# Optimization experiments

Hardware: AMD Instinct MI355X
Metric: run time of the kernel (lower is better)

Reference implementation:

```python
import jax, jax.numpy as jnp
import numpy as np

N_ATOMS = 100000
N_BONDS = 400000
ATOM_FDIM = 133
BOND_FDIM = 147
HIDDEN = 300
DEPTH = 3


def setup_inputs() -> dict:
    key = jax.random.key(0)
    ks = jax.random.split(key, 10)
    f_atoms = jax.random.normal(ks[0], (N_ATOMS, ATOM_FDIM), dtype=jnp.float32)
    f_bonds = jax.random.normal(ks[1], (N_BONDS, BOND_FDIM), dtype=jnp.float32)
    b2a = jax.random.randint(ks[2], (N_BONDS,), 0, N_ATOMS)
    b2revb = jax.random.randint(ks[3], (N_BONDS,), 0, N_BONDS)
    s_i = 1.0 / np.sqrt(BOND_FDIM)
    s_h = 1.0 / np.sqrt(HIDDEN)
    s_o = 1.0 / np.sqrt(ATOM_FDIM + HIDDEN)
    Wi_w = jax.random.uniform(ks[4], (HIDDEN, BOND_FDIM), jnp.float32, -s_i, s_i)
    Wi_b = jax.random.uniform(ks[5], (HIDDEN,), jnp.float32, -s_i, s_i)
    Wh_w = jax.random.uniform(ks[6], (HIDDEN, HIDDEN), jnp.float32, -s_h, s_h)
    Wh_b = jax.random.uniform(ks[7], (HIDDEN,), jnp.float32, -s_h, s_h)
    Wo_w = jax.random.uniform(ks[8], (HIDDEN, ATOM_FDIM + HIDDEN), jnp.float32, -s_o, s_o)
    Wo_b = jax.random.uniform(ks[9], (HIDDEN,), jnp.float32, -s_o, s_o)
    return {"f_atoms": f_atoms, "f_bonds": f_bonds, "b2a": b2a, "b2revb": b2revb,
            "Wi_w": Wi_w, "Wi_b": Wi_b, "Wh_w": Wh_w, "Wh_b": Wh_b,
            "Wo_w": Wo_w, "Wo_b": Wo_b}


def reference(f_atoms, f_bonds, b2a, b2revb, Wi_w, Wi_b, Wh_w, Wh_b, Wo_w, Wo_b):
    n_atoms = f_atoms.shape[0]
    # initial bond messages: [n_bonds, hidden]
    H_bonds = jax.nn.relu(f_bonds @ Wi_w.T + Wi_b)
    dest = b2a[b2revb]  # destination atom of each directed bond
    for _ in range(DEPTH - 1):
        # scatter-add bond messages onto destination atoms
        sum_msgs = jax.ops.segment_sum(H_bonds, dest, num_segments=n_atoms)
        # gather back to bonds from source atoms, subtract reverse-bond message
        msgs = sum_msgs[b2a] - H_bonds[b2revb]
        H_bonds = jax.nn.relu(H_bonds + msgs @ Wh_w.T + Wh_b)
    sum_msgs = jax.ops.segment_sum(H_bonds, dest, num_segments=n_atoms)
    H_atoms = jax.nn.relu(jnp.concatenate([f_atoms, sum_msgs], axis=1) @ Wo_w.T + Wo_b)
    return (H_atoms, H_bonds)
```

## Files before the change

kernel.cpp:

```cpp
#include <hip/hip_runtime.h>
#include <hip/hip_bf16.h>

#define NB 400000
#define NA 100000
#define AFD 133
#define BFD 147
#define HID 300
#define NP  320
#define SMP 304
#define NT  98

typedef short short8 __attribute__((ext_vector_type(8)));
typedef float f32x4 __attribute__((ext_vector_type(4)));

__device__ __forceinline__ ushort f2b(float f) {
    union { float f; unsigned u; } v; v.f = f;
    unsigned r = v.u + 0x7fffu + ((v.u >> 16) & 1u);
    return (ushort)(r >> 16);
}
__device__ __forceinline__ float b2f(ushort u) {
    union { unsigned u; float f; } v; v.u = ((unsigned)u) << 16;
    return v.f;
}

#define GLDS(gp, lp) __builtin_amdgcn_global_load_lds( \
    (const __attribute__((address_space(1))) void*)(gp), \
    (__attribute__((address_space(3))) void*)(lp), 16, 0, 0)


__global__ void pad_w_k(const float* __restrict__ W, ushort* __restrict__ Wp,
                        int N, int K, int Kp) {
    int idx = blockIdx.x * 256 + threadIdx.x;
    if (idx >= NP * Kp) return;
    int n = idx / Kp, k = idx - n * Kp;
    int t = k >> 5, kk = k & 31;
    int g = (kk & 15) >> 2, slot = (kk & 3) + ((kk >> 4) << 2);
    int gp = g ^ ((n >> 1) & 3);
    ushort v = (n < N && k < K) ? f2b(W[n * K + k]) : (ushort)0;
    Wp[(size_t)t * 10240 + n * 32 + gp * 8 + slot] = v;
}

__global__ void dest_k(const int* __restrict__ b2a, const int* __restrict__ b2revb,
                       int* __restrict__ dest) {
    int b = blockIdx.x * 256 + threadIdx.x;
    if (b < NB) dest[b] = b2a[b2revb[b]];
}

__global__ void count_k(const int* __restrict__ dest, int* __restrict__ cnt) {
    int b = blockIdx.x * 256 + threadIdx.x;
    if (b < NB) atomicAdd(&cnt[dest[b]], 1);
}

__global__ void scanA_k(const int* __restrict__ cnt, int* __restrict__ tsum) {
    __shared__ int sm[256];
    const int tid = threadIdx.x;
    int base = blockIdx.x * 1024 + tid * 4;
    int s = 0;
#pragma unroll
    for (int j = 0; j < 4; ++j) { int i = base + j; if (i < NA) s += cnt[i]; }
    sm[tid] = s; __syncthreads();
    for (int o = 128; o > 0; o >>= 1) {
        if (tid < o) sm[tid] += sm[tid + o];
        __syncthreads();
    }
    if (tid == 0) tsum[blockIdx.x] = sm[0];
}

__global__ void scanB_k(const int* __restrict__ tsum, int* __restrict__ toff,
                        int* __restrict__ rs) {
    if (threadIdx.x == 0) {
        int run = 0;
        for (int t = 0; t < NT; ++t) { toff[t] = run; run += tsum[t]; }
        rs[NA] = run;
    }
}

__global__ void scanC_k(const int* __restrict__ cnt, const int* __restrict__ toff,
                        int* __restrict__ rs) {
    __shared__ int sm[256];
    const int tid = threadIdx.x;
    int base = blockIdx.x * 1024 + tid * 4;
    int v[4]; int s = 0;
#pragma unroll
    for (int j = 0; j < 4; ++j) {
        v[j] = (base + j < NA) ? cnt[base + j] : 0;
        s += v[j];
    }
    sm[tid] = s; __syncthreads();
    for (int o = 1; o < 256; o <<= 1) {
        int x = (tid >= o) ? sm[tid - o] : 0;
        __syncthreads();
        sm[tid] += x;
        __syncthreads();
    }
    int acc = sm[tid] - s + toff[blockIdx.x];
#pragma unroll
    for (int j = 0; j < 4; ++j) {
        if (base + j < NA) rs[base + j] = acc;
        acc += v[j];
    }
}

__global__ void scatter_k(const int* __restrict__ dest, const int* __restrict__ rs,
                          int* __restrict__ cur, int* __restrict__ bl) {
    int b = blockIdx.x * 256 + threadIdx.x;
    if (b >= NB) return;
    int a = dest[b];
    int pos = rs[a] + atomicAdd(&cur[a], 1);
    bl[pos] = b;
}

__global__ void cvt0_k(const float* __restrict__ fb, ushort* __restrict__ Ab) {
    int idx = blockIdx.x * 256 + threadIdx.x;
    if (idx >= NB * 20) return;
    int b = idx / 20, p = idx - b * 20;
    int t = p >> 2, gp = p & 3;
    int g = gp ^ ((b >> 1) & 3);
    int k0 = t * 32 + 4 * g, k1 = k0 + 16;
    const float* src = fb + (size_t)b * BFD;
    ushort o[8];
#pragma unroll
    for (int s = 0; s < 4; ++s) o[s]     = (k0 + s < BFD) ? f2b(src[k0 + s]) : (ushort)0;
#pragma unroll
    for (int s = 0; s < 4; ++s) o[4 + s] = (k1 + s < BFD) ? f2b(src[k1 + s]) : (ushort)0;
    ushort* dst = &Ab[(size_t)b * 160 + t * 32 + gp * 8];
    *(ushort4*)dst       = make_ushort4(o[0], o[1], o[2], o[3]);
    *(ushort4*)(dst + 4) = make_ushort4(o[4], o[5], o[6], o[7]);
}

__global__ void gather_k(const float* __restrict__ sum, const ushort* __restrict__ Hb,
                         const int* __restrict__ b2a, const int* __restrict__ b2revb,
                         ushort* __restrict__ Mb) {
    int idx = blockIdx.x * 256 + threadIdx.x;
    if (idx >= NB * 40) return;
    int b = idx / 40, p = idx - b * 40;
    int t = p >> 2, gp = p & 3;
    int g = gp ^ ((b >> 1) & 3);
    int k0 = t * 32 + 4 * g, k1 = k0 + 16;
    int sa = b2a[b], rb = b2revb[b];
    const float* sp = &sum[(size_t)sa * SMP];
    const ushort* hp = &Hb[(size_t)rb * NP];
    float4 s0 = *(const float4*)&sp[k0];
    float4 s1 = (k1 < SMP) ? *(const float4*)&sp[k1] : make_float4(0.f, 0.f, 0.f, 0.f);
    ushort4 h0 = *(const ushort4*)&hp[k0];
    ushort4 h1 = *(const ushort4*)&hp[k1];
    ushort* dst = &Mb[(size_t)b * NP + t * 32 + gp * 8];
    *(ushort4*)dst       = make_ushort4(f2b(s0.x - b2f(h0.x)), f2b(s0.y - b2f(h0.y)),
                                        f2b(s0.z - b2f(h0.z)), f2b(s0.w - b2f(h0.w)));
    *(ushort4*)(dst + 4) = make_ushort4(f2b(s1.x - b2f(h1.x)), f2b(s1.y - b2f(h1.y)),
                                        f2b(s1.z - b2f(h1.z)), f2b(s1.w - b2f(h1.w)));
}

__global__ void cat2_k(const float* __restrict__ fa, const float* __restrict__ sum,
                       ushort* __restrict__ Ac) {
    int idx = blockIdx.x * 256 + threadIdx.x;
    if (idx >= NA * 56) return;
    int a = idx / 56, p = idx - a * 56;
    int t = p >> 2, gp = p & 3;
    int g = gp ^ ((a >> 1) & 3);
    ushort o[8];
#pragma unroll
    for (int e = 0; e < 8; ++e) {
        int k = t * 32 + 4 * g + (e & 3) + ((e >> 2) << 4);
        float x = 0.f;
        if (k < AFD) x = fa[(size_t)a * AFD + k];
        else if (k < AFD + HID) x = sum[(size_t)a * SMP + (k - AFD)];
        o[e] = f2b(x);
    }
    ushort* dst = &Ac[(size_t)a * 448 + t * 32 + gp * 8];
    *(ushort4*)dst       = make_ushort4(o[0], o[1], o[2], o[3]);
    *(ushort4*)(dst + 4) = make_ushort4(o[4], o[5], o[6], o[7]);
}

template<int MODE>
__global__ __launch_bounds__(512) void gemm_k(
    const ushort* __restrict__ Asrc, const ushort* __restrict__ W,
    const float* __restrict__ bias, ushort* __restrict__ Cb,
    float* __restrict__ Cf, int Kp, int Ksteps, int M)
{
    __shared__ ushort As[128 * 32];
    __shared__ ushort Bs[320 * 32];
    const int tid = threadIdx.x;
    const int w = tid >> 6, lane = tid & 63;
    const int wr = w >> 2, wc = w & 3;
    const int g = lane >> 4, lr = lane & 15;
    const int swz = (lr >> 1) & 3;
    const int m0 = blockIdx.x * 128;

    int arow = m0 + w * 16 + (lane >> 2);
    if (MODE == 2 && arow >= M) arow = M - 1;
    const ushort* aglob = Asrc + (size_t)arow * Kp + (lane & 3) * 8;
    ushort* alds = &As[w * 512];

    f32x4 acc[4][5];
#pragma unroll
    for (int mi = 0; mi < 4; ++mi)
#pragma unroll
        for (int ni = 0; ni < 5; ++ni) acc[mi][ni] = (f32x4){0.f, 0.f, 0.f, 0.f};

    for (int t = 0; t < Ksteps; ++t) {
        __syncthreads();
        GLDS(aglob + t * 32, alds);
        const ushort* wt = W + (size_t)t * 10240;
        GLDS(wt + (size_t)w * 512 + lane * 8,        &Bs[w * 512]);
        GLDS(wt + (size_t)(w + 8) * 512 + lane * 8,  &Bs[(w + 8) * 512]);
        if (w < 4)
            GLDS(wt + (size_t)(w + 16) * 512 + lane * 8, &Bs[(w + 16) * 512]);
        __syncthreads();
        short8 af[4];
#pragma unroll
        for (int mi = 0; mi < 4; ++mi) {
            int r = wr * 64 + mi * 16 + lr;
            af[mi] = *(const short8*)&As[r * 32 + ((g ^ swz) << 3)];
        }
#pragma unroll
        for (int ni = 0; ni < 5; ++ni) {
            int c = wc * 80 + ni * 16 + lr;
            short8 bf = *(const short8*)&Bs[c * 32 + ((g ^ swz) << 3)];
#pragma unroll
            for (int mi = 0; mi < 4; ++mi)
                acc[mi][ni] = __builtin_amdgcn_mfma_f32_16x16x32_bf16(af[mi], bf, acc[mi][ni], 0, 0, 0);
        }
    }
#pragma unroll
    for (int ni = 0; ni < 5; ++ni) {
        const int col = wc * 80 + ni * 16 + lr;
        const float bv = (col < HID) ? bias[col] : 0.f;
#pragma unroll
        for (int mi = 0; mi < 4; ++mi) {
            const int row = m0 + wr * 64 + mi * 16 + g * 4;
#pragma unroll
            for (int r = 0; r < 4; ++r) {
                float v = acc[mi][ni][r] + bv;
                size_t off = (size_t)(row + r) * NP + col;
                if (MODE == 1) v += b2f(Cb[off]);
                v = fmaxf(v, 0.f);
                if (MODE == 2) {
                    if (col < HID && row + r < M) Cf[(size_t)(row + r) * HID + col] = v;
                } else {
                    Cb[off] = f2b(v);
                }
            }
        }
    }
}

__global__ void seg_sum_csr_k(const ushort* __restrict__ Hb, const int* __restrict__ rs,
                              const int* __restrict__ bl, float* __restrict__ sum) {
    int idx = blockIdx.x * 256 + threadIdx.x;
    if (idx >= NA * 38) return;
    int a = idx / 38, c = (idx - a * 38) * 8;
    int s0 = rs[a], s1 = rs[a + 1];
    float acc[8] = {0.f, 0.f, 0.f, 0.f, 0.f, 0.f, 0.f, 0.f};
    for (int j = s0; j < s1; ++j) {
        const ushort* p = &Hb[(size_t)bl[j] * NP + c];
        ushort4 u0 = *(const ushort4*)p, u1 = *(const ushort4*)(p + 4);
        acc[0] += b2f(u0.x); acc[1] += b2f(u0.y);
        acc[2] += b2f(u0.z); acc[3] += b2f(u0.w);
        acc[4] += b2f(u1.x); acc[5] += b2f(u1.y);
        acc[6] += b2f(u1.z); acc[7] += b2f(u1.w);
    }
    float* dst = &sum[(size_t)a * SMP + c];
    *(float4*)dst       = make_float4(acc[0], acc[1], acc[2], acc[3]);
    *(float4*)(dst + 4) = make_float4(acc[4], acc[5], acc[6], acc[7]);
}

__global__ void conv_k(const ushort* __restrict__ Hb, float* __restrict__ out) {
    int idx = blockIdx.x * 256 + threadIdx.x;
    if (idx >= NB * 75) return;
    int b = idx / 75, c = (idx - b * 75) * 4;
    ushort4 u = *(const ushort4*)&Hb[(size_t)b * NP + c];
    float4 v = make_float4(b2f(u.x), b2f(u.y), b2f(u.z), b2f(u.w));
    *(float4*)&out[(size_t)b * HID + c] = v;
}

extern "C" void kernel_launch(void* const* d_in, const int* in_sizes, int n_in,
                              void* d_out, int out_size, void* d_ws, size_t ws_size,
                              hipStream_t stream) {
    const float* f_atoms = (const float*)d_in[0];
    const float* f_bonds = (const float*)d_in[1];
    const int*   b2a     = (const int*)d_in[2];
    const int*   b2revb  = (const int*)d_in[3];
    const float* Wi_w    = (const float*)d_in[4];
    const float* Wi_b    = (const float*)d_in[5];
    const float* Wh_w    = (const float*)d_in[6];
    const float* Wh_b    = (const float*)d_in[7];
    const float* Wo_w    = (const float*)d_in[8];
    const float* Wo_b    = (const float*)d_in[9];
    float* out = (float*)d_out;

    char* ws = (char*)d_ws;
    ushort* Hb   = (ushort*)ws;            ws += (size_t)NB * NP * 2;
    float*  sum  = (float*)ws;             ws += (size_t)NA * SMP * 4;
    int*    dest = (int*)ws;               ws += (size_t)NB * 4;
    ushort* Wp0  = (ushort*)ws;            ws += (size_t)5  * 10240 * 2;
    ushort* Wp1  = (ushort*)ws;            ws += (size_t)10 * 10240 * 2;
    ushort* Wp2  = (ushort*)ws;            ws += (size_t)14 * 10240 * 2;
    int*    cnt  = (int*)ws;               ws += (size_t)NA * 4;
    int*    cur  = (int*)ws;               ws += (size_t)NA * 4;
    int*    rs   = (int*)ws;               ws += (size_t)(NA + 1) * 4;
    int*    bl   = (int*)ws;               ws += (size_t)NB * 4;
    int*    tsum = (int*)ws;               ws += 128 * 4;
    int*    toff = (int*)ws;               ws += 128 * 4;
    float* Hatoms = out;
    float* Hbonds = out + (size_t)NA * HID;
    ushort* Mbuf  = (ushort*)Hbonds;
    ushort* Ab0   = (ushort*)((char*)Hbonds + (size_t)NB * NP * 2);
    ushort* Ac2   = Ab0;

    pad_w_k<<<(NP * 160 + 255) / 256, 256, 0, stream>>>(Wi_w, Wp0, HID, BFD, 160);
    pad_w_k<<<(NP * NP  + 255) / 256, 256, 0, stream>>>(Wh_w, Wp1, HID, HID, NP);
    pad_w_k<<<(NP * 448 + 255) / 256, 256, 0, stream>>>(Wo_w, Wp2, HID, AFD + HID, 448);
    dest_k<<<(NB + 255) / 256, 256, 0, stream>>>(b2a, b2revb, dest);
    hipMemsetAsync(cnt, 0, (size_t)NA * 4, stream);
    hipMemsetAsync(cur, 0, (size_t)NA * 4, stream);
    count_k<<<(NB + 255) / 256, 256, 0, stream>>>(dest, cnt);
    scanA_k<<<NT, 256, 0, stream>>>(cnt, tsum);
    scanB_k<<<1, 64, 0, stream>>>(tsum, toff, rs);
    scanC_k<<<NT, 256, 0, stream>>>(cnt, toff, rs);
    scatter_k<<<(NB + 255) / 256, 256, 0, stream>>>(dest, rs, cur, bl);

    cvt0_k<<<(NB * 20 + 255) / 256, 256, 0, stream>>>(f_bonds, Ab0);
    gemm_k<0><<<NB / 128, 512, 0, stream>>>(Ab0, Wp0, Wi_b, Hb, nullptr, 160, 5, NB);

    for (int it = 0; it < 2; ++it) {
        seg_sum_csr_k<<<(NA * 38 + 255) / 256, 256, 0, stream>>>(Hb, rs, bl, sum);
        gather_k<<<(NB * 40 + 255) / 256, 256, 0, stream>>>(sum, Hb, b2a, b2revb, Mbuf);
        gemm_k<1><<<NB / 128, 512, 0, stream>>>(Mbuf, Wp1, Wh_b, Hb, nullptr, NP, 10, NB);
    }

    seg_sum_csr_k<<<(NA * 38 + 255) / 256, 256, 0, stream>>>(Hb, rs, bl, sum);

    cat2_k<<<(NA * 56 + 255) / 256, 256, 0, stream>>>(f_atoms, sum, Ac2);
    gemm_k<2><<<(NA + 127) / 128, 512, 0, stream>>>(Ac2, Wp2, Wo_b, nullptr, Hatoms, 448, 14, NA);

    conv_k<<<(NB * 75 + 255) / 256, 256, 0, stream>>>(Hb, Hbonds);
}
```

Measured before the change: 1.724 ms.

## Fuse operand gather/convert into GEMM prologue and double-buffer weight tiles

```diff
diff --git a/kernel.cpp b/kernel.cpp
--- a/kernel.cpp
+++ b/kernel.cpp
@@ -110,87 +110,81 @@
     bl[pos] = b;
 }
 
-__global__ void cvt0_k(const float* __restrict__ fb, ushort* __restrict__ Ab) {
-    int idx = blockIdx.x * 256 + threadIdx.x;
-    if (idx >= NB * 20) return;
-    int b = idx / 20, p = idx - b * 20;
-    int t = p >> 2, gp = p & 3;
-    int g = gp ^ ((b >> 1) & 3);
-    int k0 = t * 32 + 4 * g, k1 = k0 + 16;
-    const float* src = fb + (size_t)b * BFD;
-    ushort o[8];
-#pragma unroll
-    for (int s = 0; s < 4; ++s) o[s]     = (k0 + s < BFD) ? f2b(src[k0 + s]) : (ushort)0;
-#pragma unroll
-    for (int s = 0; s < 4; ++s) o[4 + s] = (k1 + s < BFD) ? f2b(src[k1 + s]) : (ushort)0;
-    ushort* dst = &Ab[(size_t)b * 160 + t * 32 + gp * 8];
-    *(ushort4*)dst       = make_ushort4(o[0], o[1], o[2], o[3]);
-    *(ushort4*)(dst + 4) = make_ushort4(o[4], o[5], o[6], o[7]);
-}
-
-__global__ void gather_k(const float* __restrict__ sum, const ushort* __restrict__ Hb,
-                         const int* __restrict__ b2a, const int* __restrict__ b2revb,
-                         ushort* __restrict__ Mb) {
-    int idx = blockIdx.x * 256 + threadIdx.x;
-    if (idx >= NB * 40) return;
-    int b = idx / 40, p = idx - b * 40;
-    int t = p >> 2, gp = p & 3;
-    int g = gp ^ ((b >> 1) & 3);
-    int k0 = t * 32 + 4 * g, k1 = k0 + 16;
-    int sa = b2a[b], rb = b2revb[b];
-    const float* sp = &sum[(size_t)sa * SMP];
-    const ushort* hp = &Hb[(size_t)rb * NP];
-    float4 s0 = *(const float4*)&sp[k0];
-    float4 s1 = (k1 < SMP) ? *(const float4*)&sp[k1] : make_float4(0.f, 0.f, 0.f, 0.f);
-    ushort4 h0 = *(const ushort4*)&hp[k0];
-    ushort4 h1 = *(const ushort4*)&hp[k1];
-    ushort* dst = &Mb[(size_t)b * NP + t * 32 + gp * 8];
-    *(ushort4*)dst       = make_ushort4(f2b(s0.x - b2f(h0.x)), f2b(s0.y - b2f(h0.y)),
-                                        f2b(s0.z - b2f(h0.z)), f2b(s0.w - b2f(h0.w)));
-    *(ushort4*)(dst + 4) = make_ushort4(f2b(s1.x - b2f(h1.x)), f2b(s1.y - b2f(h1.y)),
-                                        f2b(s1.z - b2f(h1.z)), f2b(s1.w - b2f(h1.w)));
-}
-
-__global__ void cat2_k(const float* __restrict__ fa, const float* __restrict__ sum,
-                       ushort* __restrict__ Ac) {
-    int idx = blockIdx.x * 256 + threadIdx.x;
-    if (idx >= NA * 56) return;
-    int a = idx / 56, p = idx - a * 56;
-    int t = p >> 2, gp = p & 3;
-    int g = gp ^ ((a >> 1) & 3);
-    ushort o[8];
-#pragma unroll
-    for (int e = 0; e < 8; ++e) {
-        int k = t * 32 + 4 * g + (e & 3) + ((e >> 2) << 4);
-        float x = 0.f;
-        if (k < AFD) x = fa[(size_t)a * AFD + k];
-        else if (k < AFD + HID) x = sum[(size_t)a * SMP + (k - AFD)];
-        o[e] = f2b(x);
-    }
-    ushort* dst = &Ac[(size_t)a * 448 + t * 32 + gp * 8];
-    *(ushort4*)dst       = make_ushort4(o[0], o[1], o[2], o[3]);
-    *(ushort4*)(dst + 4) = make_ushort4(o[4], o[5], o[6], o[7]);
-}
-
-template<int MODE>
+template<int MODE, bool OUTF>
 __global__ __launch_bounds__(512) void gemm_k(
-    const ushort* __restrict__ Asrc, const ushort* __restrict__ W,
-    const float* __restrict__ bias, ushort* __restrict__ Cb,
-    float* __restrict__ Cf, int Kp, int Ksteps, int M)
+    const float* __restrict__ F1, const float* __restrict__ Sum,
+    const ushort* __restrict__ HbIn,
+    const int* __restrict__ b2a, const int* __restrict__ b2revb,
+    const ushort* __restrict__ W, const float* __restrict__ bias,
+    ushort* __restrict__ Cb, float* __restrict__ Cf, int M)
 {
-    __shared__ ushort As[128 * 32];
-    __shared__ ushort Bs[320 * 32];
+    constexpr int KP = (MODE == 0) ? 192 : (MODE == 1) ? 320 : 448;
+    constexpr int TILES = KP / 32;
+    static_assert(KP % 64 == 0 && TILES % 2 == 0, "XOR swizzle needs 128B-mult rows, even tiles");
+    __shared__ ushort As[128 * KP];
+    __shared__ ushort Bs[2][320 * 32];
+
     const int tid = threadIdx.x;
     const int w = tid >> 6, lane = tid & 63;
     const int wr = w >> 2, wc = w & 3;
     const int g = lane >> 4, lr = lane & 15;
-    const int swz = (lr >> 1) & 3;
     const int m0 = blockIdx.x * 128;
 
-    int arow = m0 + w * 16 + (lane >> 2);
-    if (MODE == 2 && arow >= M) arow = M - 1;
-    const ushort* aglob = Asrc + (size_t)arow * Kp + (lane & 3) * 8;
-    ushort* alds = &As[w * 512];
+    {
+        const int row = tid >> 2, q = tid & 3;
+        int grow = m0 + row;
+        if (MODE == 2 && grow >= M) grow = M - 1;
+        const int axw = (row & 7) << 4;
+        char* abase = (char*)As + (size_t)row * (KP * 2);
+        const float* sp = nullptr; const ushort* hp = nullptr;
+        if (MODE == 1) {
+            sp = Sum + (size_t)b2a[grow] * SMP;
+            hp = HbIn + (size_t)b2revb[grow] * NP;
+        }
+#pragma unroll
+        for (int t = 0; t < TILES; ++t) {
+            const int k0 = t * 32 + 4 * q, k1 = k0 + 16;
+            ushort o[8];
+            if (MODE == 0) {
+                const float* src = F1 + (size_t)grow * BFD;
+#pragma unroll
+                for (int s = 0; s < 4; ++s) o[s]     = (k0 + s < BFD) ? f2b(src[k0 + s]) : (ushort)0;
+#pragma unroll
+                for (int s = 0; s < 4; ++s) o[4 + s] = (k1 + s < BFD) ? f2b(src[k1 + s]) : (ushort)0;
+            } else if (MODE == 1) {
+                float4 s0 = *(const float4*)(sp + k0);
+                float4 s1 = (k1 < SMP) ? *(const float4*)(sp + k1)
+                                       : make_float4(0.f, 0.f, 0.f, 0.f);
+                ushort4 h0 = *(const ushort4*)(hp + k0);
+                ushort4 h1 = *(const ushort4*)(hp + k1);
+                o[0] = f2b(s0.x - b2f(h0.x)); o[1] = f2b(s0.y - b2f(h0.y));
+                o[2] = f2b(s0.z - b2f(h0.z)); o[3] = f2b(s0.w - b2f(h0.w));
+                o[4] = f2b(s1.x - b2f(h1.x)); o[5] = f2b(s1.y - b2f(h1.y));
+                o[6] = f2b(s1.z - b2f(h1.z)); o[7] = f2b(s1.w - b2f(h1.w));
+            } else {
+#pragma unroll
+                for (int s = 0; s < 8; ++s) {
+                    int k = (s < 4) ? (k0 + s) : (k1 + s - 4);
+                    float x = 0.f;
+                    if (k < AFD) x = F1[(size_t)grow * AFD + k];
+                    else if (k < AFD + HID) x = Sum[(size_t)grow * SMP + (k - AFD)];
+                    o[s] = f2b(x);
+                }
+            }
+            ushort* dst = (ushort*)(abase + ((t * 64 + q * 16) ^ axw));
+            *(ushort4*)dst       = make_ushort4(o[0], o[1], o[2], o[3]);
+            *(ushort4*)(dst + 4) = make_ushort4(o[4], o[5], o[6], o[7]);
+        }
+    }
+
+    auto stageB = [&](int t, int buf) {
+        const ushort* wt = W + (size_t)t * 10240;
+        ushort* bs = &Bs[buf][0];
+        GLDS(wt + (size_t)w * 512 + lane * 8,        bs + w * 512);
+        GLDS(wt + (size_t)(w + 8) * 512 + lane * 8,  bs + (w + 8) * 512);
+        if (w < 4)
+            GLDS(wt + (size_t)(w + 16) * 512 + lane * 8, bs + (w + 16) * 512);
+    };
 
     f32x4 acc[4][5];
 #pragma unroll
@@ -198,47 +192,50 @@
 #pragma unroll
         for (int ni = 0; ni < 5; ++ni) acc[mi][ni] = (f32x4){0.f, 0.f, 0.f, 0.f};
 
-    for (int t = 0; t < Ksteps; ++t) {
-        __syncthreads();
-        GLDS(aglob + t * 32, alds);
-        const ushort* wt = W + (size_t)t * 10240;
-        GLDS(wt + (size_t)w * 512 + lane * 8,        &Bs[w * 512]);
-        GLDS(wt + (size_t)(w + 8) * 512 + lane * 8,  &Bs[(w + 8) * 512]);
-        if (w < 4)
-            GLDS(wt + (size_t)(w + 16) * 512 + lane * 8, &Bs[(w + 16) * 512]);
-        __syncthreads();
+    stageB(0, 0);
+    __syncthreads();
+
+    const int raxw = (lr & 7) << 4;
+    const int bswz = ((lr >> 1) & 3);
+    for (int t = 0; t < TILES; ++t) {
+        if (t + 1 < TILES) stageB(t + 1, (t + 1) & 1);
+        const ushort* bs = &Bs[t & 1][0];
         short8 af[4];
 #pragma unroll
         for (int mi = 0; mi < 4; ++mi) {
-            int r = wr * 64 + mi * 16 + lr;
-            af[mi] = *(const short8*)&As[r * 32 + ((g ^ swz) << 3)];
+            const int r = wr * 64 + mi * 16 + lr;
+            af[mi] = *(const short8*)((const char*)As + (size_t)r * (KP * 2)
+                                      + ((t * 64 + g * 16) ^ raxw));
         }
 #pragma unroll
         for (int ni = 0; ni < 5; ++ni) {
-            int c = wc * 80 + ni * 16 + lr;
-            short8 bf = *(const short8*)&Bs[c * 32 + ((g ^ swz) << 3)];
+            const int c = wc * 80 + ni * 16 + lr;
+            short8 bf = *(const short8*)&bs[c * 32 + ((g ^ bswz) << 3)];
 #pragma unroll
             for (int mi = 0; mi < 4; ++mi)
                 acc[mi][ni] = __builtin_amdgcn_mfma_f32_16x16x32_bf16(af[mi], bf, acc[mi][ni], 0, 0, 0);
         }
-    }
+        __syncthreads();
+    }
+
 #pragma unroll
     for (int ni = 0; ni < 5; ++ni) {
         const int col = wc * 80 + ni * 16 + lr;
         const float bv = (col < HID) ? bias[col] : 0.f;
 #pragma unroll
         for (int mi = 0; mi < 4; ++mi) {
-            const int row = m0 + wr * 64 + mi * 16 + g * 4;
+            const int row0 = m0 + wr * 64 + mi * 16 + g * 4;
 #pragma unroll
             for (int r = 0; r < 4; ++r) {
+                const int row = row0 + r;
                 float v = acc[mi][ni][r] + bv;
-                size_t off = (size_t)(row + r) * NP + col;
-                if (MODE == 1) v += b2f(Cb[off]);
+                if (MODE == 1) v += b2f(HbIn[(size_t)row * NP + col]);
                 v = fmaxf(v, 0.f);
                 if (MODE == 2) {
-                    if (col < HID && row + r < M) Cf[(size_t)(row + r) * HID + col] = v;
+                    if (col < HID && row < M) Cf[(size_t)row * HID + col] = v;
                 } else {
-                    Cb[off] = f2b(v);
+                    Cb[(size_t)row * NP + col] = f2b(v);
+                    if (OUTF && col < HID) Cf[(size_t)row * HID + col] = v;
                 }
             }
         }
@@ -265,15 +262,6 @@
     *(float4*)(dst + 4) = make_float4(acc[4], acc[5], acc[6], acc[7]);
 }
 
-__global__ void conv_k(const ushort* __restrict__ Hb, float* __restrict__ out) {
-    int idx = blockIdx.x * 256 + threadIdx.x;
-    if (idx >= NB * 75) return;
-    int b = idx / 75, c = (idx - b * 75) * 4;
-    ushort4 u = *(const ushort4*)&Hb[(size_t)b * NP + c];
-    float4 v = make_float4(b2f(u.x), b2f(u.y), b2f(u.z), b2f(u.w));
-    *(float4*)&out[(size_t)b * HID + c] = v;
-}
-
 extern "C" void kernel_launch(void* const* d_in, const int* in_sizes, int n_in,
                               void* d_out, int out_size, void* d_ws, size_t ws_size,
                               hipStream_t stream) {
@@ -290,10 +278,11 @@
     float* out = (float*)d_out;
 
     char* ws = (char*)d_ws;
-    ushort* Hb   = (ushort*)ws;            ws += (size_t)NB * NP * 2;
+    ushort* HbA  = (ushort*)ws;            ws += (size_t)NB * NP * 2;
+    ushort* HbB  = (ushort*)ws;            ws += (size_t)NB * NP * 2;
     float*  sum  = (float*)ws;             ws += (size_t)NA * SMP * 4;
     int*    dest = (int*)ws;               ws += (size_t)NB * 4;
-    ushort* Wp0  = (ushort*)ws;            ws += (size_t)5  * 10240 * 2;
+    ushort* Wp0  = (ushort*)ws;            ws += (size_t)6  * 10240 * 2;
     ushort* Wp1  = (ushort*)ws;            ws += (size_t)10 * 10240 * 2;
     ushort* Wp2  = (ushort*)ws;            ws += (size_t)14 * 10240 * 2;
     int*    cnt  = (int*)ws;               ws += (size_t)NA * 4;
@@ -304,11 +293,8 @@
     int*    toff = (int*)ws;               ws += 128 * 4;
     float* Hatoms = out;
     float* Hbonds = out + (size_t)NA * HID;
-    ushort* Mbuf  = (ushort*)Hbonds;
-    ushort* Ab0   = (ushort*)((char*)Hbonds + (size_t)NB * NP * 2);
-    ushort* Ac2   = Ab0;
-
-    pad_w_k<<<(NP * 160 + 255) / 256, 256, 0, stream>>>(Wi_w, Wp0, HID, BFD, 160);
+
+    pad_w_k<<<(NP * 192 + 255) / 256, 256, 0, stream>>>(Wi_w, Wp0, HID, BFD, 192);
     pad_w_k<<<(NP * NP  + 255) / 256, 256, 0, stream>>>(Wh_w, Wp1, HID, HID, NP);
     pad_w_k<<<(NP * 448 + 255) / 256, 256, 0, stream>>>(Wo_w, Wp2, HID, AFD + HID, 448);
     dest_k<<<(NB + 255) / 256, 256, 0, stream>>>(b2a, b2revb, dest);
@@ -320,19 +306,18 @@
     scanC_k<<<NT, 256, 0, stream>>>(cnt, toff, rs);
     scatter_k<<<(NB + 255) / 256, 256, 0, stream>>>(dest, rs, cur, bl);
 
-    cvt0_k<<<(NB * 20 + 255) / 256, 256, 0, stream>>>(f_bonds, Ab0);
-    gemm_k<0><<<NB / 128, 512, 0, stream>>>(Ab0, Wp0, Wi_b, Hb, nullptr, 160, 5, NB);
-
-    for (int it = 0; it < 2; ++it) {
-        seg_sum_csr_k<<<(NA * 38 + 255) / 256, 256, 0, stream>>>(Hb, rs, bl, sum);
-        gather_k<<<(NB * 40 + 255) / 256, 256, 0, stream>>>(sum, Hb, b2a, b2revb, Mbuf);
-        gemm_k<1><<<NB / 128, 512, 0, stream>>>(Mbuf, Wp1, Wh_b, Hb, nullptr, NP, 10, NB);
-    }
-
-    seg_sum_csr_k<<<(NA * 38 + 255) / 256, 256, 0, stream>>>(Hb, rs, bl, sum);
-
-    cat2_k<<<(NA * 56 + 255) / 256, 256, 0, stream>>>(f_atoms, sum, Ac2);
-    gemm_k<2><<<(NA + 127) / 128, 512, 0, stream>>>(Ac2, Wp2, Wo_b, nullptr, Hatoms, 448, 14, NA);
-
-    conv_k<<<(NB * 75 + 255) / 256, 256, 0, stream>>>(Hb, Hbonds);
-}
+    gemm_k<0, false><<<NB / 128, 512, 0, stream>>>(
+        f_bonds, nullptr, nullptr, nullptr, nullptr, Wp0, Wi_b, HbA, nullptr, NB);
+
+    seg_sum_csr_k<<<(NA * 38 + 255) / 256, 256, 0, stream>>>(HbA, rs, bl, sum);
+    gemm_k<1, false><<<NB / 128, 512, 0, stream>>>(
+        nullptr, sum, HbA, b2a, b2revb, Wp1, Wh_b, HbB, nullptr, NB);
+
+    seg_sum_csr_k<<<(NA * 38 + 255) / 256, 256, 0, stream>>>(HbB, rs, bl, sum);
+    gemm_k<1, true><<<NB / 128, 512, 0, stream>>>(
+        nullptr, sum, HbB, b2a, b2revb, Wp1, Wh_b, HbA, Hbonds, NB);
+
+    seg_sum_csr_k<<<(NA * 38 + 255) / 256, 256, 0, stream>>>(HbA, rs, bl, sum);
+    gemm_k<2, false><<<(NA + 127) / 128, 512, 0, stream>>>(
+        f_atoms, sum, nullptr, nullptr, nullptr, Wp2, Wo_b, nullptr, Hatoms, NA);
+}
```

New measurement: 1.808 ms. 1.05x slower.
